# Optimization experiments

Hardware: AMD Instinct MI355X
Metric: run time of the kernel (lower is better)

Reference implementation:

```python
import jax, jax.numpy as jnp
import numpy as np

B, T, V = 128, 128, 30000
DE, DP, PV = 300, 30, 50
H = 300
HEADS = 6
LA, LL = 5, 24
POL = 3
RED = 10
NEG = -1e9


def entmax15(x):
    # exact 1.5-entmax along last axis (sorting algorithm, Peters & Martins 2019)
    d = x.shape[-1]
    x = x / 2.0
    x = x - jnp.max(x, axis=-1, keepdims=True)
    xs = -jnp.sort(-x, axis=-1)                      # descending
    rho = jnp.arange(1, d + 1, dtype=x.dtype)
    mean = jnp.cumsum(xs, axis=-1) / rho
    meansq = jnp.cumsum(xs * xs, axis=-1) / rho
    ss = rho * (meansq - mean * mean)
    delta = (1.0 - ss) / rho
    tau = mean - jnp.sqrt(jnp.maximum(delta, 0.0))
    support = jnp.sum((tau <= xs).astype(jnp.int32), axis=-1, keepdims=True)
    tau_star = jnp.take_along_axis(tau, support - 1, axis=-1)
    return jnp.square(jnp.maximum(x - tau_star, 0.0))


def lstm_dir(x, mask, Wih, Whh, bih, bhh, reverse):
    # packed-sequence-equivalent LSTM: state frozen / output zeroed at padded steps
    b = x.shape[0]
    h0 = jnp.zeros((b, Whh.shape[1]), x.dtype)

    def step(carry, inp):
        h, c = carry
        xt, mt = inp
        g = xt @ Wih.T + h @ Whh.T + (bih + bhh)
        i, f, gg, o = jnp.split(g, 4, axis=-1)       # torch gate order i,f,g,o
        c_new = jax.nn.sigmoid(f) * c + jax.nn.sigmoid(i) * jnp.tanh(gg)
        h_new = jax.nn.sigmoid(o) * jnp.tanh(c_new)
        m = mt[:, None]
        return (jnp.where(m, h_new, h), jnp.where(m, c_new, c)), jnp.where(m, h_new, 0.0)

    _, outs = jax.lax.scan(step, (h0, h0),
                           (jnp.swapaxes(x, 0, 1), jnp.swapaxes(mask, 0, 1)),
                           reverse=reverse)
    return jnp.swapaxes(outs, 0, 1)


def se_layer(x, valid, w1, b1, w2, b2):
    # SELayer over the SEQUENCE dim (channel == max_len); x: [b,t,d], valid: [b,t]
    y = jnp.mean(x, axis=-1)                         # adaptive avg-pool over (1, d)
    y = jax.nn.relu(y @ w1.T + b1) @ w2.T + b2
    y = y + jnp.where(valid > 0, 0.0, NEG)           # mask_2
    y = jax.nn.softmax(y, axis=1)
    return x * y[..., None]


def gcn(x, A, W, b):
    # D @ A @ D @ x @ W + b with D = diag((rowsum(A)+1)^-0.5)
    dn = (jnp.sum(A, axis=2) + 1.0) ** -0.5
    An = dn[:, :, None] * A * dn[:, None, :]
    return jnp.einsum('bij,bjd->bid', An, x) @ W + b


def _forward(text_indices, aspect_indices, left_indices, pos_indices, asp_post, height,
             adj, embed_matrix, pos_emb_w, Wih_f, Whh_f, bih_f, bhh_f,
             Wih_b, Whh_b, bih_b, bhh_b, wq, bq, wk, bk,
             se_w1, se_b1, se_w2, se_b2, gc1_w, gc1_b, gc2_w, gc2_b,
             affine1, affine2, fc_w, fc_b):
    b, t = text_indices.shape
    nonpad = text_indices != 0
    valid = nonpad.astype(jnp.float32)               # mask_ squeezed -> [b,t]
    text_len = jnp.sum(nonpad, axis=-1)
    aspect_real_len = jnp.sum(aspect_indices != 0, axis=-1)
    left_len = jnp.sum(left_indices != 0, axis=-1)   # aspect_double_idx = [left_len,left_len]

    # embedding; overwrite aspect position with mean aspect embedding
    text = embed_matrix[text_indices]
    am = (aspect_indices != 0).astype(jnp.float32)[..., None]
    asp_mean = jnp.sum(embed_matrix[aspect_indices] * am, axis=1) / aspect_real_len[:, None].astype(jnp.float32)
    text = text.at[jnp.arange(b), asp_post].set(asp_mean)
    embs = jnp.concatenate([text, pos_emb_w[pos_indices]], axis=-1)

    lenmask = jnp.arange(t)[None, :] < text_len[:, None]
    text_out = jnp.concatenate([
        lstm_dir(embs, lenmask, Wih_f, Whh_f, bih_f, bhh_f, False),
        lstm_dir(embs, lenmask, Wih_b, Whh_b, bih_b, bhh_b, True)], axis=-1)  # [b,t,2H]

    # multi-head entmax attention -> semantic adjacency
    dk = (2 * H) // HEADS
    q = (text_out @ wq.T + bq).reshape(b, t, HEADS, dk).transpose(0, 2, 1, 3)
    k = (text_out @ wk.T + bk).reshape(b, t, HEADS, dk).transpose(0, 2, 1, 3)
    scores = jnp.einsum('bhqd,bhkd->bhqk', q, k) / (dk ** 0.5)
    scores = jnp.where(nonpad[:, None, None, :], scores, NEG)
    adj_sem = jnp.mean(entmax15(scores), axis=1)     # average over heads
    eye = jnp.eye(t, dtype=adj_sem.dtype)
    adj_sem = adj_sem * (1.0 - eye) + eye            # zero diagonal, add identity
    adj_sem = valid[:, :, None] * adj_sem

    se = lambda z: se_layer(z, valid, se_w1, se_b1, se_w2, se_b2)
    # (the first x = relu(gc1(..,adj)); x = relu(gc2(..,adj)) branch is dead code:
    #  x is overwritten before use, so only the x_sem path matters)
    x_sem = jax.nn.relu(gcn(se(text_out), adj_sem, gc1_w, gc1_b))
    x = jax.nn.relu(gcn(se(x_sem), adj, gc2_w, gc2_b))

    A1 = jax.nn.softmax(jnp.einsum('bid,bjd->bij', x @ affine1, x_sem), axis=-1)
    A2 = jax.nn.softmax(jnp.einsum('bid,bjd->bij', x_sem @ affine2, x), axis=-1)
    out = jnp.concatenate([jnp.einsum('bij,bjd->bid', A1, x_sem),
                           jnp.einsum('bij,bjd->bid', A2, x)], axis=-1)  # [b,t,4H]
    aspmask = (jnp.arange(t)[None, :] == left_len[:, None]).astype(jnp.float32)
    pooled = jnp.sum(out * aspmask[..., None], axis=1)  # keep aspect token only
    return pooled @ fc_w + fc_b                         # [b, POL]


def setup_inputs():
    key = jax.random.key(0)
    ks = jax.random.split(key, 36)
    f32 = jnp.float32
    pos_t = jnp.arange(T)[None, :]
    text_len = jax.random.randint(ks[0], (B,), T // 2, T + 1)
    text_indices = jax.random.randint(ks[1], (B, T), 1, V) * (pos_t < text_len[:, None])
    asp_len = jax.random.randint(ks[2], (B,), 1, LA + 1)
    aspect_indices = jax.random.randint(ks[3], (B, LA), 1, V) * (jnp.arange(LA)[None, :] < asp_len[:, None])
    left_len = jax.random.randint(ks[4], (B,), 1, LL + 1)
    left_indices = jax.random.randint(ks[5], (B, LL), 1, V) * (jnp.arange(LL)[None, :] < left_len[:, None])
    pos_indices = jax.random.randint(ks[6], (B, T), 1, PV) * (pos_t < text_len[:, None])
    vmask = (pos_t < text_len[:, None]).astype(f32)
    adj = (jax.random.uniform(ks[7], (B, T, T)) < 0.08).astype(f32)
    adj = adj * vmask[:, :, None] * vmask[:, None, :]
    asp_post = left_len                              # aspect sits right after left context
    height = jax.random.randint(ks[8], (B, T + 1), 1, 12)

    def rn(k, shape, scale=0.05):
        return jax.random.normal(k, shape, dtype=f32) * scale

    params = dict(
        embed_matrix=rn(ks[9], (V, DE), 0.5),
        pos_emb_w=rn(ks[10], (PV, DP), 0.5).at[0].set(0.0),
        Wih_f=rn(ks[11], (4 * H, DE + DP)), Whh_f=rn(ks[12], (4 * H, H)),
        bih_f=rn(ks[13], (4 * H,)), bhh_f=rn(ks[14], (4 * H,)),
        Wih_b=rn(ks[15], (4 * H, DE + DP)), Whh_b=rn(ks[16], (4 * H, H)),
        bih_b=rn(ks[17], (4 * H,)), bhh_b=rn(ks[18], (4 * H,)),
        wq=rn(ks[19], (2 * H, 2 * H)), bq=rn(ks[20], (2 * H,)),
        wk=rn(ks[21], (2 * H, 2 * H)), bk=rn(ks[22], (2 * H,)),
        se_w1=rn(ks[23], (T // RED, T)), se_b1=rn(ks[24], (T // RED,)),
        se_w2=rn(ks[25], (T, T // RED)), se_b2=rn(ks[26], (T,)),
        gc1_w=rn(ks[27], (2 * H, 2 * H)), gc1_b=rn(ks[28], (2 * H,)),
        gc2_w=rn(ks[29], (2 * H, 2 * H)), gc2_b=rn(ks[30], (2 * H,)),
        affine1=rn(ks[31], (2 * H, 2 * H)), affine2=rn(ks[32], (2 * H, 2 * H)),
        fc_w=rn(ks[33], (4 * H, POL)), fc_b=rn(ks[34], (POL,)),
    )
    return dict(text_indices=text_indices, aspect_indices=aspect_indices,
                left_indices=left_indices, pos_indices=pos_indices,
                asp_post=asp_post, height=height, adj=adj, **params)


def reference(text_indices, aspect_indices, left_indices, pos_indices, asp_post, height,
              adj, embed_matrix, pos_emb_w, Wih_f, Whh_f, bih_f, bhh_f,
              Wih_b, Whh_b, bih_b, bhh_b, wq, bq, wk, bk,
              se_w1, se_b1, se_w2, se_b2, gc1_w, gc1_b, gc2_w, gc2_b,
              affine1, affine2, fc_w, fc_b):
    return _forward(text_indices, aspect_indices, left_indices, pos_indices, asp_post, height,
                    adj, embed_matrix, pos_emb_w, Wih_f, Whh_f, bih_f, bhh_f,
                    Wih_b, Whh_b, bih_b, bhh_b, wq, bq, wk, bk,
                    se_w1, se_b1, se_w2, se_b2, gc1_w, gc1_b, gc2_w, gc2_b,
                    affine1, affine2, fc_w, fc_b)
```

## Files before the change

kernel.cpp:

```cpp
#include <hip/hip_runtime.h>

typedef unsigned short ushort_t;
typedef unsigned int   uint_t;
typedef __attribute__((ext_vector_type(8))) short short8;
typedef __attribute__((ext_vector_type(4))) float floatx4;

#define NEGV -1000000000.0f

__device__ __forceinline__ float bf2f(ushort_t h){ return __uint_as_float(((uint_t)h)<<16); }
__device__ __forceinline__ ushort_t f2bf(float f){
  uint_t u = __float_as_uint(f);
  uint_t r = u + 0x7fffu + ((u>>16)&1u);
  return (ushort_t)(r>>16);
}
__device__ __forceinline__ float wredsum(float v){ for(int o=32;o;o>>=1) v += __shfl_xor(v,o); return v; }
__device__ __forceinline__ float wredmax(float v){ for(int o=32;o;o>>=1) v = fmaxf(v,__shfl_xor(v,o)); return v; }
__device__ __forceinline__ int   wredsumi(int v){ for(int o=32;o;o>>=1) v += __shfl_xor(v,o); return v; }

__device__ __forceinline__ short8 ldg_cohr(const ushort_t* p){
  short8 r;
  asm volatile("global_load_dwordx4 %0, %1, off sc0 sc1"
               : "=&v"(r) : "v"(p) : "memory");
  return r;
}
__device__ __forceinline__ void stg_b128_cohr(ushort_t* p, short8 v){
  asm volatile("global_store_dwordx4 %0, %1, off sc0 sc1" :: "v"(p), "v"(v) : "memory");
}

__device__ __forceinline__ float fsig(float x){ return 1.f/(1.f+__expf(-x)); }
__device__ __forceinline__ float ftanh(float x){ return 1.f - 2.f/(1.f+__expf(2.f*x)); }

__global__ void k_cvt8(const void* __restrict__ src, ushort_t* __restrict__ dst,
                       long n, const ushort_t* __restrict__ probe_src){
  __shared__ int sflag;
  if (threadIdx.x < 64){
    ushort_t u = probe_src[2*threadIdx.x];
    int e = (u>>7)&0xFF;
    int c = (e>=100 && e<=140) ? 1 : 0;
    c = wredsumi(c);
    if (threadIdx.x==0) sflag = (c>32) ? 1 : 0;
  }
  __syncthreads();
  bool isbf = (sflag!=0);
  long base = (blockIdx.x*256L + threadIdx.x)*8;
  if (base>=n) return;
  if (isbf){
    if (base+8<=n) *(uint4*)(dst+base) = *(const uint4*)((const ushort_t*)src+base);
    else for (long i=base;i<n;i++) dst[i]=((const ushort_t*)src)[i];
  } else {
    const float* s = (const float*)src;
    if (base+8<=n){
      float4 v0 = *(const float4*)(s+base);
      float4 v1 = *(const float4*)(s+base+4);
      ushort_t o[8] = {f2bf(v0.x),f2bf(v0.y),f2bf(v0.z),f2bf(v0.w),
                       f2bf(v1.x),f2bf(v1.y),f2bf(v1.z),f2bf(v1.w)};
      *(uint4*)(dst+base) = *(uint4*)o;
    } else {
      for (long i=base;i<n;i++) dst[i]=f2bf(s[i]);
    }
  }
}

__device__ __forceinline__ bool probe_is_bf16(const ushort_t* probe_src){
  int c=0;
  #pragma unroll 1
  for (int i=0;i<64;i++){
    ushort_t u = probe_src[2*i];
    int e = (u>>7)&0xFF;
    c += (e>=100 && e<=140) ? 1 : 0;
  }
  return c>32;
}

__global__ void k_lens(const int* __restrict__ ti, const int* __restrict__ li,
                       int* __restrict__ nonpad, int* __restrict__ text_len,
                       int* __restrict__ left_len){
  int b = blockIdx.x, t = threadIdx.x;
  nonpad[b*128+t] = (ti[b*128+t]!=0) ? 1 : 0;
  if (t==0){
    int c=0; for (int k2=0;k2<128;k2++) c += (ti[b*128+k2]!=0);
    text_len[b]=c;
    int l=0; for (int k2=0;k2<24;k2++) l += (li[b*24+k2]!=0);
    left_len[b]=l;
  }
}

__global__ void k_aspmean(const int* __restrict__ ai, const ushort_t* __restrict__ em,
                          float* __restrict__ asp_mean){
  int b = blockIdx.x;
  int idxs[5]; int cnt=0;
  for (int a=0;a<5;a++){ int ix=ai[b*5+a]; idxs[a]=ix; cnt += (ix!=0); }
  float inv = 1.0f/(float)cnt;
  for (int d=threadIdx.x; d<300; d+=128){
    float s=0.f;
    for (int a=0;a<5;a++) if (idxs[a]) s += bf2f(em[(long)idxs[a]*300+d]);
    asp_mean[b*300+d] = s*inv;
  }
}

__global__ void k_embs(const int* __restrict__ ti, const int* __restrict__ pi,
                       const int* __restrict__ asp_post,
                       const ushort_t* __restrict__ em, const ushort_t* __restrict__ pe,
                       const float* __restrict__ asp_mean, ushort_t* __restrict__ embs){
  int blk = blockIdx.x;
  int b = blk>>7, t = blk&127;
  int ap = asp_post[b];
  int tix = ti[b*128+t];
  int pix = pi[b*128+t];
  for (int col=threadIdx.x; col<336; col+=128){
    ushort_t v;
    if (col<300) v = (t==ap) ? f2bf(asp_mean[b*300+col]) : em[(long)tix*300+col];
    else if (col<330) v = pe[pix*30 + (col-300)];
    else v = 0;
    embs[(long)(b*128+t)*336 + col] = v;
  }
}

__global__ void k_padwih2(const ushort_t* __restrict__ src, ushort_t* __restrict__ dst){
  int i = blockIdx.x*blockDim.x + threadIdx.x;
  if (i >= 1280*336) return;
  int r = i/336, k = i - r*336;
  int j = r>>2, gate = r&3;
  ushort_t v = 0;
  if (j<300 && k<330) v = src[(long)(gate*300+j)*330 + k];
  dst[i] = v;
}

__global__ void k_padwhh2(const ushort_t* __restrict__ src, ushort_t* __restrict__ dst){
  int i = blockIdx.x*blockDim.x + threadIdx.x;
  if (i >= 1280*320) return;
  int r = i/320, k = i - r*320;
  int j = r>>2, gate = r&3;
  ushort_t v = 0;
  if (j<300 && k<300) v = src[(long)(gate*300+j)*300 + k];
  dst[i] = v;
}

__global__ void k_biassum2(const ushort_t* __restrict__ a, const ushort_t* __restrict__ b,
                           float* __restrict__ dst){
  int i = blockIdx.x*blockDim.x + threadIdx.x;
  if (i>=1280) return;
  int j = i>>2, g = i&3;
  dst[i] = (j<300) ? (bf2f(a[g*300+j]) + bf2f(b[g*300+j])) : 0.f;
}

__global__ void k_biascvt(const ushort_t* __restrict__ a, float* __restrict__ dst, int n){
  int i = blockIdx.x*blockDim.x + threadIdx.x;
  if (i<n) dst[i] = bf2f(a[i]);
}

template<int TB, int MODE>
__global__ __launch_bounds__(256) void gemm_k(
    int M, int N, int K,
    const ushort_t* __restrict__ A, long lda, long sAz,
    const ushort_t* __restrict__ B, long ldb, long sBz,
    float* __restrict__ Cf, ushort_t* __restrict__ Cb, long ldc, long sCz,
    const float* __restrict__ bias, int relu,
    const float* __restrict__ rowscale,
    const int* __restrict__ nonpad)
{
  __shared__ ushort_t As[128*40];
  __shared__ ushort_t Bs[128*40];
  const int tid = threadIdx.x;
  const int m0 = blockIdx.x*128, n0 = blockIdx.y*128;
  const int z = blockIdx.z;
  const ushort_t* Ap = A + (long)z*sAz;
  const ushort_t* Bp = B + (long)z*sBz;
  floatx4 acc[4][4];
  #pragma unroll
  for (int i=0;i<4;i++)
    #pragma unroll
    for (int j=0;j<4;j++){ acc[i][j][0]=0.f; acc[i][j][1]=0.f; acc[i][j][2]=0.f; acc[i][j][3]=0.f; }
  const int w = tid>>6, wm = w&1, wn = w>>1;
  const int lane = tid&63, lr = lane&15, lq = lane>>4;

  for (int k0=0;k0<K;k0+=32){
    #pragma unroll
    for (int c2=0;c2<2;c2++){
      int ch = tid + 256*c2;
      int row = ch>>2, kc = (ch&3)*8;
      int gr = m0+row, gk = k0+kc;
      uint4 v{};
      if (gr<M && gk<K) v = *(const uint4*)(Ap + (long)gr*lda + gk);
      *(uint4*)(&As[row*40+kc]) = v;
    }
    if (TB){
      #pragma unroll
      for (int c2=0;c2<2;c2++){
        int ch = tid + 256*c2;
        int row = ch>>2, kc = (ch&3)*8;
        int gn = n0+row, gk = k0+kc;
        uint4 v{};
        if (gn<N && gk<K) v = *(const uint4*)(Bp + (long)gn*ldb + gk);
        int sw = kc ^ (((row>>3)&3)<<3);
        *(uint4*)(&Bs[row*40+sw]) = v;
      }
    } else {
      #pragma unroll
      for (int c2=0;c2<2;c2++){
        int ch = tid + 256*c2;
        int kk = ch>>4, nc = (ch&15)*8;
        int gk = k0+kk, gn = n0+nc;
        uint4 v{};
        if (gk<K && gn<N) v = *(const uint4*)(Bp + (long)gk*ldb + gn);
        uint_t wsv[4] = {v.x, v.y, v.z, v.w};
        #pragma unroll
        for (int e=0;e<8;e++){
          ushort_t hv = (e&1) ? (ushort_t)(wsv[e>>1]>>16) : (ushort_t)(wsv[e>>1]&0xffffu);
          int n = nc+e;
          int sw = kk ^ (((n>>3)&3)<<3);
          Bs[n*40+sw] = hv;
        }
      }
    }
    __syncthreads();
    short8 af[4], bfv[4];
    #pragma unroll
    for (int i=0;i<4;i++) af[i] = *(const short8*)(&As[(wm*64+i*16+lr)*40 + lq*8]);
    #pragma unroll
    for (int j=0;j<4;j++){
      int n = wn*64+j*16+lr;
      int sw = (lq*8) ^ (((n>>3)&3)<<3);
      bfv[j] = *(const short8*)(&Bs[n*40+sw]);
    }
    #pragma unroll
    for (int i=0;i<4;i++)
      #pragma unroll
      for (int j=0;j<4;j++)
        acc[i][j] = __builtin_amdgcn_mfma_f32_16x16x32_bf16(af[i], bfv[j], acc[i][j], 0,0,0);
    __syncthreads();
  }

  #pragma unroll
  for (int i=0;i<4;i++){
    #pragma unroll
    for (int j=0;j<4;j++){
      #pragma unroll
      for (int r=0;r<4;r++){
        int row = m0 + wm*64 + i*16 + lq*4 + r;
        int col = n0 + wn*64 + j*16 + lr;
        if (row<M && col<N){
          float v = acc[i][j][r];
          if (rowscale) v *= rowscale[(long)z*M + row];
          if (bias) v += bias[col];
          if (relu && v<0.f) v = 0.f;
          if (MODE==1){
            Cb[(long)z*sCz + (long)row*ldc + col] = f2bf(v);
          } else if (MODE==2){
            int b = row>>7, t = row&127;
            int h = col/100, d = col - h*100;
            Cb[ ((long)((b*6+h)*128+t))*104 + d ] = f2bf(v);
          } else if (MODE==3){
            v *= 0.1f;
            if (!nonpad[(z/6)*128 + col]) v = NEGV;
            Cf[(long)z*sCz + (long)row*ldc + col] = v;
          }
        }
      }
    }
  }
}

#define BLD 328
#define HXD 40

__global__ __launch_bounds__(512,1) void lstm2_k(
    const ushort_t* __restrict__ whh2f, const ushort_t* __restrict__ whh2b,
    const ushort_t* __restrict__ gipf, const ushort_t* __restrict__ gipb,
    ushort_t* __restrict__ hbuf,
    int* __restrict__ barr,
    ushort_t* __restrict__ text_out, const int* __restrict__ text_len,
    ushort_t* __restrict__ dumpb)
{
  __shared__ ushort_t Blds[64*BLD];
  __shared__ ushort_t hx[64*HXD];

  const int bx = blockIdx.x;
  const int slice = bx % 10;
  const int grp   = bx / 10;
  const int dir = grp & 1, bh = grp >> 1;
  const ushort_t* __restrict__ whh = dir ? whh2b : whh2f;
  const ushort_t* __restrict__ gip = dir ? gipb : gipf;
  ushort_t* hb = hbuf + (long)dir * (2L*128*320);
  int* bar = barr + grp*128;

  const int tid = threadIdx.x;
  const int w = tid>>6, lane = tid&63, lr = lane&15, lq = lane>>4;
  const int wm = w&3, wn = w>>2;

  short8 a[2][10];
  #pragma unroll
  for (int mi=0;mi<2;mi++){
    const ushort_t* ar = whh + (long)(slice*128 + (wm*2+mi)*16 + lr)*320 + lq*8;
    #pragma unroll
    for (int kf=0;kf<10;kf++) a[mi][kf] = *(const short8*)(ar + kf*32);
  }
  #pragma unroll
  for (int mi=0;mi<2;mi++)
    #pragma unroll
    for (int kf=0;kf<10;kf++)
      asm volatile("" : "+v"(a[mi][kf]));

  int jj_[2], b_[2], bl_[2], tl_[2];
  #pragma unroll
  for (int mi=0;mi<2;mi++) jj_[mi] = slice*32 + wm*8 + mi*4 + lq;
  #pragma unroll
  for (int ni=0;ni<2;ni++){
    bl_[ni] = wn*32 + ni*16 + lr;
    b_[ni]  = bh*64 + bl_[ni];
    tl_[ni] = text_len[b_[ni]];
  }

  const int boff0 = (wn*32+   lr)*BLD + lq*8;
  const int boff1 = (wn*32+16+lr)*BLD + lq*8;

  float    c_st[2][2];
  ushort_t h_st[2][2];
  #pragma unroll
  for (int mi=0;mi<2;mi++){ c_st[mi][0]=0.f; c_st[mi][1]=0.f; h_st[mi][0]=0; h_st[mi][1]=0; }

  uint2 gp[2][2];
  {
    int t0 = dir ? 127 : 0;
    #pragma unroll
    for (int mi=0;mi<2;mi++)
      #pragma unroll
      for (int ni=0;ni<2;ni++)
        gp[mi][ni] = *(const uint2*)(gip + ((long)(b_[ni]*128 + t0))*1280 + jj_[mi]*4);
  }

  for (int s=0; s<128; s++){
    const int t = dir ? (127-s) : s;
    const ushort_t* rb = hb + (long)(s&1)*(128L*320);
    ushort_t*       wb = hb + (long)((s+1)&1)*(128L*320);

    short8 tmp[5]; int ro_[5], ch_[5];
    #pragma unroll
    for (int k=0;k<5;k++){
      int c = tid + k*512;
      int row = c/40, ch = c - row*40;
      ro_[k]=row; ch_[k]=ch;
      tmp[k] = ldg_cohr(rb + (long)(bh*64+row)*320 + ch*8);
    }
    asm volatile("s_waitcnt vmcnt(0)" ::: "memory");
    __builtin_amdgcn_sched_barrier(0);
    #pragma unroll
    for (int k=0;k<5;k++)
      *(short8*)(&Blds[ro_[k]*BLD + ch_[k]*8]) = tmp[k];
    __syncthreads();

    floatx4 acc[2][2];
    #pragma unroll
    for (int mi=0;mi<2;mi++)
      #pragma unroll
      for (int ni=0;ni<2;ni++){ acc[mi][ni][0]=0.f; acc[mi][ni][1]=0.f; acc[mi][ni][2]=0.f; acc[mi][ni][3]=0.f; }
    #pragma unroll
    for (int kf=0;kf<10;kf++){
      short8 b0 = *(const short8*)(&Blds[boff0 + kf*32]);
      short8 b1 = *(const short8*)(&Blds[boff1 + kf*32]);
      acc[0][0] = __builtin_amdgcn_mfma_f32_16x16x32_bf16(a[0][kf], b0, acc[0][0], 0,0,0);
      acc[0][1] = __builtin_amdgcn_mfma_f32_16x16x32_bf16(a[0][kf], b1, acc[0][1], 0,0,0);
      acc[1][0] = __builtin_amdgcn_mfma_f32_16x16x32_bf16(a[1][kf], b0, acc[1][0], 0,0,0);
      acc[1][1] = __builtin_amdgcn_mfma_f32_16x16x32_bf16(a[1][kf], b1, acc[1][1], 0,0,0);
    }

    ushort_t tov[2][2];
    #pragma unroll
    for (int mi=0;mi<2;mi++){
      #pragma unroll
      for (int ni=0;ni<2;ni++){
        float g_i = acc[mi][ni][0] + bf2f((ushort_t)(gp[mi][ni].x & 0xffffu));
        float g_f = acc[mi][ni][1] + bf2f((ushort_t)(gp[mi][ni].x >> 16));
        float g_g = acc[mi][ni][2] + bf2f((ushort_t)(gp[mi][ni].y & 0xffffu));
        float g_o = acc[mi][ni][3] + bf2f((ushort_t)(gp[mi][ni].y >> 16));
        float ig = fsig(g_i);
        float fg = fsig(g_f);
        float gg = ftanh(g_g);
        float og = fsig(g_o);
        float cn = fg*c_st[mi][ni] + ig*gg;
        float hn = og*ftanh(cn);
        bool m = (t < tl_[ni]);
        if (m) c_st[mi][ni] = cn;
        ushort_t hv = m ? f2bf(hn) : h_st[mi][ni];
        h_st[mi][ni] = hv;
        hx[bl_[ni]*HXD + wm*8 + mi*4 + lq] = hv;
        tov[mi][ni] = m ? f2bf(hn) : (ushort_t)0;
      }
    }
    __syncthreads();

    if (tid < 256){
      int row = tid>>2, jj8 = (tid&3)*8;
      short8 hvv = *(const short8*)(&hx[row*HXD + jj8]);
      stg_b128_cohr(wb + (long)(bh*64+row)*320 + slice*32 + jj8, hvv);
    }
    #pragma unroll
    for (int mi=0;mi<2;mi++)
      #pragma unroll
      for (int ni=0;ni<2;ni++){
        ushort_t* toa = (jj_[mi] < 300)
          ? &text_out[((long)(b_[ni]*128 + t))*600 + dir*300 + jj_[mi]]
          : &dumpb[tid*4 + mi*2 + ni];
        *toa = tov[mi][ni];
      }
    {
      int tn = dir ? ((s<127) ? (126-s) : 127) : ((s<127) ? (s+1) : 0);
      #pragma unroll
      for (int mi=0;mi<2;mi++)
        #pragma unroll
        for (int ni=0;ni<2;ni++)
          gp[mi][ni] = *(const uint2*)(gip + ((long)(b_[ni]*128 + tn))*1280 + jj_[mi]*4);
    }
    asm volatile("s_waitcnt vmcnt(8)" ::: "memory");
    __syncthreads();
    if (tid==0){
      __hip_atomic_fetch_add(&bar[s], 1, __ATOMIC_RELAXED, __HIP_MEMORY_SCOPE_AGENT);
      while (__hip_atomic_load(&bar[s], __ATOMIC_RELAXED, __HIP_MEMORY_SCOPE_AGENT) < 10)
        __builtin_amdgcn_s_sleep(1);
    }
    __syncthreads();
  }
}

__global__ __launch_bounds__(64) void k_entmax(float* __restrict__ p){
  long row = blockIdx.x;
  float* base = p + row*128;
  __shared__ float xo[128], xs[128], c1[128], c2[128];
  int t = threadIdx.x;
  float a = base[t]*0.5f, b = base[t+64]*0.5f;
  float m = wredmax(fmaxf(a,b));
  a -= m; b -= m;
  xo[t]=a; xo[t+64]=b; xs[t]=a; xs[t+64]=b;
  __syncthreads();
  for (int k2=2;k2<=128;k2<<=1){
    for (int j=k2>>1;j>0;j>>=1){
      int i = ((t & ~(j-1))<<1) | (t & (j-1));
      int ixj = i | j;
      float vi = xs[i], vj = xs[ixj];
      bool blk = (i & k2)==0;
      bool sw = blk ? (vi < vj) : (vi > vj);
      __syncthreads();
      if (sw){ xs[i]=vj; xs[ixj]=vi; }
      __syncthreads();
    }
  }
  c1[t]=xs[t];       c2[t]=xs[t]*xs[t];
  c1[t+64]=xs[t+64]; c2[t+64]=xs[t+64]*xs[t+64];
  __syncthreads();
  for (int d=1; d<128; d<<=1){
    float a1 = (t>=d)     ? c1[t-d]    : 0.f;
    float a2 = (t>=d)     ? c2[t-d]    : 0.f;
    float b1 = (t+64>=d)  ? c1[t+64-d] : 0.f;
    float b2 = (t+64>=d)  ? c2[t+64-d] : 0.f;
    float x1=c1[t], y1=c2[t], x2=c1[t+64], y2=c2[t+64];
    __syncthreads();
    c1[t]=x1+a1; c2[t]=y1+a2; c1[t+64]=x2+b1; c2[t+64]=y2+b2;
    __syncthreads();
  }
  float tau_a, tau_b; int cnt=0;
  {
    float rho = (float)(t+1);
    float mean = c1[t]/rho, msq = c2[t]/rho;
    float ss = rho*(msq-mean*mean);
    float delta = (1.f-ss)/rho;
    tau_a = mean - sqrtf(fmaxf(delta,0.f));
    cnt += (tau_a <= xs[t]) ? 1 : 0;
  }
  {
    float rho = (float)(t+65);
    float mean = c1[t+64]/rho, msq = c2[t+64]/rho;
    float ss = rho*(msq-mean*mean);
    float delta = (1.f-ss)/rho;
    tau_b = mean - sqrtf(fmaxf(delta,0.f));
    cnt += (tau_b <= xs[t+64]) ? 1 : 0;
  }
  __syncthreads();
  c1[t]=tau_a; c1[t+64]=tau_b;
  __syncthreads();
  int support = wredsumi(cnt);
  support = (support<1) ? 1 : ((support>128) ? 128 : support);
  float tau_star = c1[support-1];
  float oa = fmaxf(xo[t]-tau_star, 0.f);
  float ob = fmaxf(xo[t+64]-tau_star, 0.f);
  base[t] = oa*oa; base[t+64] = ob*ob;
}

__global__ void k_adjsem(const float* __restrict__ p, const int* __restrict__ nonpad,
                         ushort_t* __restrict__ adj_sem){
  int idx = blockIdx.x*blockDim.x + threadIdx.x;
  if (idx >= 128*128*128) return;
  int b = idx>>14, rem = idx&16383, i = rem>>7, j = rem&127;
  float s = 0.f;
  for (int h=0;h<6;h++) s += p[(long)b*98304 + h*16384 + i*128 + j];
  float v = s/6.0f;
  if (i==j) v = 1.0f;
  if (!nonpad[b*128+i]) v = 0.f;
  adj_sem[idx] = f2bf(v);
}

__global__ __launch_bounds__(64) void k_dn(const ushort_t* __restrict__ src, float* __restrict__ dnv){
  long row = blockIdx.x;
  int l = threadIdx.x;
  float s = bf2f(src[row*128+l]) + bf2f(src[row*128+l+64]);
  s = wredsum(s);
  if (l==0) dnv[row] = 1.0f/sqrtf(s+1.0f);
}

__global__ __launch_bounds__(64) void k_mean(const ushort_t* __restrict__ X, float* __restrict__ ymean){
  long row = blockIdx.x;
  float s=0.f;
  for (int d=threadIdx.x; d<600; d+=64) s += bf2f(X[row*600+d]);
  s = wredsum(s);
  if (threadIdx.x==0) ymean[row] = s/600.0f;
}

__global__ void k_senet(const float* __restrict__ ymean,
                        const ushort_t* __restrict__ w1, const ushort_t* __restrict__ b1,
                        const ushort_t* __restrict__ w2, const ushort_t* __restrict__ b2,
                        const int* __restrict__ nonpad, float* __restrict__ ysoft){
  int b = blockIdx.x, t = threadIdx.x;
  __shared__ float yv[128], z1[12], red[128];
  yv[t] = ymean[b*128+t];
  __syncthreads();
  if (t<12){
    float s = bf2f(b1[t]);
    for (int k2=0;k2<128;k2++) s += yv[k2]*bf2f(w1[t*128+k2]);
    z1[t] = fmaxf(s,0.f);
  }
  __syncthreads();
  float v = bf2f(b2[t]);
  for (int r=0;r<12;r++) v += z1[r]*bf2f(w2[t*12+r]);
  if (!nonpad[b*128+t]) v += NEGV;
  red[t]=v; __syncthreads();
  for (int s2=64;s2>0;s2>>=1){ if (t<s2) red[t]=fmaxf(red[t],red[t+s2]); __syncthreads(); }
  float mx = red[0]; __syncthreads();
  float e = expf(v-mx);
  red[t]=e; __syncthreads();
  for (int s2=64;s2>0;s2>>=1){ if (t<s2) red[t]+=red[t+s2]; __syncthreads(); }
  float sm = red[0];
  ysoft[b*128+t] = e/sm;
}

__global__ void k_scale2(const ushort_t* __restrict__ X, const float* __restrict__ ysoft,
                         const float* __restrict__ dnv, ushort_t* __restrict__ out){
  int i = blockIdx.x*blockDim.x + threadIdx.x;
  if (i >= 128*128*600) return;
  int row = i/600;
  out[i] = f2bf(bf2f(X[i])*ysoft[row]*dnv[row]);
}

__global__ void k_gather(const ushort_t* __restrict__ X, const int* __restrict__ left_len,
                         ushort_t* __restrict__ dst){
  int b = blockIdx.x;
  int lb = left_len[b];
  for (int d=threadIdx.x; d<600; d+=128)
    dst[b*600+d] = X[(long)(b*128+lb)*600+d];
}

__global__ __launch_bounds__(256) void k_pool(const ushort_t* __restrict__ g,
                                              const ushort_t* __restrict__ X,
                                              float* __restrict__ pooled, int poff){
  int b = blockIdx.x, tid = threadIdx.x;
  __shared__ float gs[600], sbuf[128], red[256];
  for (int d=tid; d<600; d+=256) gs[d] = bf2f(g[b*600+d]);
  __syncthreads();
  int wv = tid>>6, lane = tid&63;
  for (int jj=wv; jj<128; jj+=4){
    float s=0.f;
    for (int d=lane; d<600; d+=64) s += gs[d]*bf2f(X[(long)(b*128+jj)*600+d]);
    s = wredsum(s);
    if (lane==0) sbuf[jj]=s;
  }
  __syncthreads();
  float v = (tid<128) ? sbuf[tid] : -3.4e38f;
  red[tid]=v; __syncthreads();
  for (int s2=128;s2>0;s2>>=1){ if (tid<s2) red[tid]=fmaxf(red[tid],red[tid+s2]); __syncthreads(); }
  float mx = red[0]; __syncthreads();
  float e = (tid<128) ? expf(v-mx) : 0.f;
  red[tid]=e; __syncthreads();
  for (int s2=128;s2>0;s2>>=1){ if (tid<s2) red[tid]+=red[tid+s2]; __syncthreads(); }
  float sm = red[0]; __syncthreads();
  if (tid<128) sbuf[tid] = e/sm;
  __syncthreads();
  for (int d=tid; d<600; d+=256){
    float acc=0.f;
    for (int j=0;j<128;j++) acc += sbuf[j]*bf2f(X[(long)(b*128+j)*600+d]);
    pooled[(long)b*1200 + poff + d] = acc;
  }
}

__global__ __launch_bounds__(64) void k_final(const float* __restrict__ pooled,
                                              const ushort_t* __restrict__ fcw,
                                              const ushort_t* __restrict__ fcb,
                                              void* __restrict__ out,
                                              const ushort_t* __restrict__ probe_src){
  bool isbf = probe_is_bf16(probe_src);
  int b = blockIdx.x, lane = threadIdx.x;
  for (int p=0;p<3;p++){
    float s=0.f;
    for (int d=lane; d<1200; d+=64) s += pooled[(long)b*1200+d]*bf2f(fcw[d*3+p]);
    s = wredsum(s);
    if (lane==0){
      float r = s + bf2f(fcb[p]);
      if (isbf) ((ushort_t*)out)[b*3+p] = f2bf(r);
      else      ((float*)out)[b*3+p] = r;
    }
  }
}

extern "C" void kernel_launch(void* const* d_in, const int* in_sizes, int n_in,
                              void* d_out, int out_size, void* d_ws, size_t ws_size,
                              hipStream_t stream) {
  const int*      ti   = (const int*)d_in[0];
  const int*      ai   = (const int*)d_in[1];
  const int*      li   = (const int*)d_in[2];
  const int*      pi   = (const int*)d_in[3];
  const int*      aps  = (const int*)d_in[4];
  const ushort_t* probe = (const ushort_t*)d_in[7];

  char* w = (char*)d_ws; size_t off = 0;
  auto alloc = [&](size_t bytes)->char*{ char* p = w+off; off = (off+bytes+255)&~(size_t)255; return p; };

  int*   text_len = (int*)alloc(512);
  int*   left_len = (int*)alloc(512);
  int*   nonpad   = (int*)alloc(65536);
  float* asp_mean = (float*)alloc(153600);
  float* dn1      = (float*)alloc(65536);
  float* dn2      = (float*)alloc(65536);
  float* ymean    = (float*)alloc(65536);
  float* ysoft    = (float*)alloc(65536);
  ushort_t* wihpf = (ushort_t*)alloc(860160);
  ushort_t* wihpb = (ushort_t*)alloc(860160);
  ushort_t* whh2f = (ushort_t*)alloc(819200);
  ushort_t* whh2b = (ushort_t*)alloc(819200);
  ushort_t* hbuf  = (ushort_t*)alloc(327680);
  int*      barr  = (int*)alloc(2048);
  ushort_t* dumpb = (ushort_t*)alloc(4096);
  float* biasgf   = (float*)alloc(5120);
  float* biasgb   = (float*)alloc(5120);
  float* bqf      = (float*)alloc(2400);
  float* bkf      = (float*)alloc(2400);
  float* gc1bf    = (float*)alloc(2400);
  float* gc2bf    = (float*)alloc(2400);
  ushort_t* g1    = (ushort_t*)alloc(153600);
  ushort_t* g2    = (ushort_t*)alloc(153600);
  ushort_t* xr    = (ushort_t*)alloc(153600);
  ushort_t* xsr   = (ushort_t*)alloc(153600);
  float* pooled   = (float*)alloc(614400);
  ushort_t* adj_c  = (ushort_t*)alloc(4194304);
  ushort_t* pe_c   = (ushort_t*)alloc(2048);
  ushort_t* wihf_c = (ushort_t*)alloc(792000);
  ushort_t* wihb_c = (ushort_t*)alloc(792000);
  ushort_t* whhf_c = (ushort_t*)alloc(720000);
  ushort_t* whhb_c = (ushort_t*)alloc(720000);
  ushort_t* bihf_c = (ushort_t*)alloc(2400);
  ushort_t* bhhf_c = (ushort_t*)alloc(2400);
  ushort_t* bihb_c = (ushort_t*)alloc(2400);
  ushort_t* bhhb_c = (ushort_t*)alloc(2400);
  ushort_t* wq_c   = (ushort_t*)alloc(720000);
  ushort_t* bq_c   = (ushort_t*)alloc(1200);
  ushort_t* wk_c   = (ushort_t*)alloc(720000);
  ushort_t* bk_c   = (ushort_t*)alloc(1200);
  ushort_t* sw1_c  = (ushort_t*)alloc(3072);
  ushort_t* sb1_c  = (ushort_t*)alloc(256);
  ushort_t* sw2_c  = (ushort_t*)alloc(3072);
  ushort_t* sb2_c  = (ushort_t*)alloc(256);
  ushort_t* g1w_c  = (ushort_t*)alloc(720000);
  ushort_t* g1b_c  = (ushort_t*)alloc(1200);
  ushort_t* g2w_c  = (ushort_t*)alloc(720000);
  ushort_t* g2b_c  = (ushort_t*)alloc(1200);
  ushort_t* af1_c  = (ushort_t*)alloc(720000);
  ushort_t* af2_c  = (ushort_t*)alloc(720000);
  ushort_t* fcw_c  = (ushort_t*)alloc(7200);
  ushort_t* fcb_c  = (ushort_t*)alloc(256);
  ushort_t* embs  = (ushort_t*)alloc(11010048);
  ushort_t* textout = (ushort_t*)alloc(19660800);
  char* R = alloc(95420416);
  ushort_t* em_c    = (ushort_t*)(R);
  ushort_t* gip_f   = (ushort_t*)(R);
  ushort_t* gip_b   = (ushort_t*)(R+41943040);
  ushort_t* qh      = (ushort_t*)(R);
  ushort_t* kh      = (ushort_t*)(R+20447232);
  float*    scores  = (float*)(R+40894464);
  ushort_t* adj_sem = (ushort_t*)(R+91226112);
  ushort_t* se_x    = (ushort_t*)(R+40894464);
  ushort_t* Zb      = (ushort_t*)(R+60555264);
  ushort_t* x_sem   = (ushort_t*)(R);
  ushort_t* xb      = (ushort_t*)(R+20447232);
  (void)ws_size; (void)n_in; (void)in_sizes; (void)out_size;

  {
    const int idx[27] = {7,6, 8,9,13,10,14,11,12,15,16,17,18,19,20,21,22,23,24,25,26,27,28,29,30,31,32};
    ushort_t* dl[27] = {em_c,adj_c, pe_c,wihf_c,wihb_c,whhf_c,whhb_c,bihf_c,bhhf_c,bihb_c,bhhb_c,
                        wq_c,bq_c,wk_c,bk_c,sw1_c,sb1_c,sw2_c,sb2_c,
                        g1w_c,g1b_c,g2w_c,g2b_c,af1_c,af2_c,fcw_c,fcb_c};
    const long nl[27] = {9000000L,2097152L, 900,396000,396000,360000,360000,1200,1200,1200,1200,
                         360000,600,360000,600,1536,12,1536,128,
                         360000,600,360000,600,360000,360000,3600,3};
    for (int i=0;i<27;i++){
      long nb = ((nl[i]+7)/8 + 255)/256;
      k_cvt8<<<(int)nb,256,0,stream>>>(d_in[idx[i]], dl[i], nl[i], probe);
    }
  }

  k_lens<<<128,128,0,stream>>>(ti, li, nonpad, text_len, left_len);
  k_aspmean<<<128,128,0,stream>>>(ai, em_c, asp_mean);
  k_embs<<<16384,128,0,stream>>>(ti, pi, aps, em_c, pe_c, asp_mean, embs);
  k_padwih2<<<(1280*336+255)/256,256,0,stream>>>(wihf_c, wihpf);
  k_padwih2<<<(1280*336+255)/256,256,0,stream>>>(wihb_c, wihpb);
  k_padwhh2<<<(1280*320+255)/256,256,0,stream>>>(whhf_c, whh2f);
  k_padwhh2<<<(1280*320+255)/256,256,0,stream>>>(whhb_c, whh2b);
  k_biassum2<<<(1280+255)/256,256,0,stream>>>(bihf_c, bhhf_c, biasgf);
  k_biassum2<<<(1280+255)/256,256,0,stream>>>(bihb_c, bhhb_c, biasgb);
  k_biascvt<<<3,256,0,stream>>>(bq_c, bqf, 600);
  k_biascvt<<<3,256,0,stream>>>(bk_c, bkf, 600);
  k_biascvt<<<3,256,0,stream>>>(g1b_c, gc1bf, 600);
  k_biascvt<<<3,256,0,stream>>>(g2b_c, gc2bf, 600);

  gemm_k<1,1><<<dim3(128,10,1),256,0,stream>>>(16384,1280,336, embs,336,0, wihpf,336,0,
        nullptr, gip_f,1280,0, biasgf,0,nullptr,nullptr);
  gemm_k<1,1><<<dim3(128,10,1),256,0,stream>>>(16384,1280,336, embs,336,0, wihpb,336,0,
        nullptr, gip_b,1280,0, biasgb,0,nullptr,nullptr);

  hipMemsetAsync(hbuf, 0, 327680, stream);
  hipMemsetAsync(barr, 0, 2048, stream);
  lstm2_k<<<40,512,0,stream>>>(whh2f, whh2b, gip_f, gip_b, hbuf, barr, textout, text_len, dumpb);

  hipMemsetAsync(qh, 0, 20447232, stream);
  hipMemsetAsync(kh, 0, 20447232, stream);
  gemm_k<1,2><<<dim3(128,5,1),256,0,stream>>>(16384,600,600, textout,600,0, wq_c,600,0,
        nullptr, qh,0,0, bqf,0,nullptr,nullptr);
  gemm_k<1,2><<<dim3(128,5,1),256,0,stream>>>(16384,600,600, textout,600,0, wk_c,600,0,
        nullptr, kh,0,0, bkf,0,nullptr,nullptr);

  gemm_k<1,3><<<dim3(1,1,768),256,0,stream>>>(128,128,104, qh,104,13312, kh,104,13312,
        scores, nullptr, 128, 16384, nullptr,0,nullptr, nonpad);

  k_entmax<<<98304,64,0,stream>>>(scores);

  k_adjsem<<<(2097152+255)/256,256,0,stream>>>(scores, nonpad, adj_sem);
  k_dn<<<16384,64,0,stream>>>(adj_sem, dn1);
  k_dn<<<16384,64,0,stream>>>(adj_c, dn2);

  k_mean<<<16384,64,0,stream>>>(textout, ymean);
  k_senet<<<128,128,0,stream>>>(ymean, sw1_c,sb1_c,sw2_c,sb2_c, nonpad, ysoft);
  k_scale2<<<(9830400+255)/256,256,0,stream>>>(textout, ysoft, dn1, se_x);
  gemm_k<0,1><<<dim3(1,5,128),256,0,stream>>>(128,600,128, adj_sem,128,16384, se_x,600,76800,
        nullptr, Zb,600,76800, nullptr,0, dn1, nullptr);
  gemm_k<0,1><<<dim3(128,5,1),256,0,stream>>>(16384,600,600, Zb,600,0, g1w_c,600,0,
        nullptr, x_sem,600,0, gc1bf,1,nullptr,nullptr);

  k_mean<<<16384,64,0,stream>>>(x_sem, ymean);
  k_senet<<<128,128,0,stream>>>(ymean, sw1_c,sb1_c,sw2_c,sb2_c, nonpad, ysoft);
  k_scale2<<<(9830400+255)/256,256,0,stream>>>(x_sem, ysoft, dn2, se_x);
  gemm_k<0,1><<<dim3(1,5,128),256,0,stream>>>(128,600,128, adj_c,128,16384, se_x,600,76800,
        nullptr, Zb,600,76800, nullptr,0, dn2, nullptr);
  gemm_k<0,1><<<dim3(128,5,1),256,0,stream>>>(16384,600,600, Zb,600,0, g2w_c,600,0,
        nullptr, xb,600,0, gc2bf,1,nullptr,nullptr);

  k_gather<<<128,128,0,stream>>>(xb, left_len, xr);
  k_gather<<<128,128,0,stream>>>(x_sem, left_len, xsr);
  gemm_k<0,1><<<dim3(1,5,1),256,0,stream>>>(128,600,600, xr,600,0, af1_c,600,0,
        nullptr, g1,600,0, nullptr,0,nullptr,nullptr);
  gemm_k<0,1><<<dim3(1,5,1),256,0,stream>>>(128,600,600, xsr,600,0, af2_c,600,0,
        nullptr, g2,600,0, nullptr,0,nullptr,nullptr);
  k_pool<<<128,256,0,stream>>>(g1, x_sem, pooled, 0);
  k_pool<<<128,256,0,stream>>>(g2, xb, pooled, 600);

  k_final<<<128,64,0,stream>>>(pooled, fcw_c, fcb_c, d_out, probe);
}
```

Baseline: 1.865 ms.

## Batch small weight conversions, use per-slice flags for LSTM barrier, zero only pad columns

Merges 25 small conversion launches into one multi-tensor kernel indexed by blockIdx.y. The LSTM inter-block barrier changes from an atomic counter polled by thread 0 plus a second syncthreads to per-slice flag stores that every wave polls directly. The full memsets of the q/k head buffers are replaced by a kernel that zeroes only the four pad columns per row. The aims are fewer launches, lower per-step barrier latency in the recurrent loop, and less memset traffic. The risk is that waves polling independently read h before the other slices have published it, if memory ordering is not preserved.

```diff
diff --git a/kernel.cpp b/kernel.cpp
--- a/kernel.cpp
+++ b/kernel.cpp
@@ -61,6 +61,42 @@
   }
 }
 
+struct CvtTab { const void* src[25]; ushort_t* dst[25]; long n[25]; };
+
+__global__ void k_cvt8_multi(CvtTab tab, const ushort_t* __restrict__ probe_src){
+  __shared__ int sflag;
+  if (threadIdx.x < 64){
+    ushort_t u = probe_src[2*threadIdx.x];
+    int e = (u>>7)&0xFF;
+    int c = (e>=100 && e<=140) ? 1 : 0;
+    c = wredsumi(c);
+    if (threadIdx.x==0) sflag = (c>32) ? 1 : 0;
+  }
+  __syncthreads();
+  bool isbf = (sflag!=0);
+  int ix = blockIdx.y;
+  long n = tab.n[ix];
+  long base = (blockIdx.x*256L + threadIdx.x)*8;
+  if (base>=n) return;
+  const void* src = tab.src[ix];
+  ushort_t* dst = tab.dst[ix];
+  if (isbf){
+    if (base+8<=n) *(uint4*)(dst+base) = *(const uint4*)((const ushort_t*)src+base);
+    else for (long i=base;i<n;i++) dst[i]=((const ushort_t*)src)[i];
+  } else {
+    const float* s = (const float*)src;
+    if (base+8<=n){
+      float4 v0 = *(const float4*)(s+base);
+      float4 v1 = *(const float4*)(s+base+4);
+      ushort_t o[8] = {f2bf(v0.x),f2bf(v0.y),f2bf(v0.z),f2bf(v0.w),
+                       f2bf(v1.x),f2bf(v1.y),f2bf(v1.z),f2bf(v1.w)};
+      *(uint4*)(dst+base) = *(uint4*)o;
+    } else {
+      for (long i=base;i<n;i++) dst[i]=f2bf(s[i]);
+    }
+  }
+}
+
 __device__ __forceinline__ bool probe_is_bf16(const ushort_t* probe_src){
   int c=0;
   #pragma unroll 1
@@ -147,6 +183,15 @@
 __global__ void k_biascvt(const ushort_t* __restrict__ a, float* __restrict__ dst, int n){
   int i = blockIdx.x*blockDim.x + threadIdx.x;
   if (i<n) dst[i] = bf2f(a[i]);
+}
+
+__global__ void k_padzero(ushort_t* __restrict__ qh, ushort_t* __restrict__ kh){
+  int i = blockIdx.x*blockDim.x + threadIdx.x;
+  if (i >= 98304*4*2) return;
+  int half = (i >= 98304*4) ? 1 : 0;
+  int j = i - half*98304*4;
+  int row = j>>2, c = 100 + (j&3);
+  (half ? kh : qh)[(long)row*104 + c] = 0;
 }
 
 template<int TB, int MODE>
@@ -282,7 +327,7 @@
   const ushort_t* __restrict__ whh = dir ? whh2b : whh2f;
   const ushort_t* __restrict__ gip = dir ? gipb : gipf;
   ushort_t* hb = hbuf + (long)dir * (2L*128*320);
-  int* bar = barr + grp*128;
+  int* flg = barr + grp*160;
 
   const int tid = threadIdx.x;
   const int w = tid>>6, lane = tid&63, lr = lane&15, lq = lane>>4;
@@ -413,12 +458,19 @@
     }
     asm volatile("s_waitcnt vmcnt(8)" ::: "memory");
     __syncthreads();
-    if (tid==0){
-      __hip_atomic_fetch_add(&bar[s], 1, __ATOMIC_RELAXED, __HIP_MEMORY_SCOPE_AGENT);
-      while (__hip_atomic_load(&bar[s], __ATOMIC_RELAXED, __HIP_MEMORY_SCOPE_AGENT) < 10)
-        __builtin_amdgcn_s_sleep(1);
-    }
-    __syncthreads();
+
+    if (tid==0)
+      __hip_atomic_store(&flg[slice*16], s+1, __ATOMIC_RELAXED, __HIP_MEMORY_SCOPE_AGENT);
+    {
+      bool done = false;
+      do {
+        int f = 0x7fffffff;
+        if (lane < 10)
+          f = __hip_atomic_load(&flg[lane*16], __ATOMIC_RELAXED, __HIP_MEMORY_SCOPE_AGENT);
+        done = (bool)__all(f >= s+1);
+        if (!done) __builtin_amdgcn_s_sleep(1);
+      } while(!done);
+    }
   }
 }
 
@@ -634,7 +686,7 @@
   ushort_t* whh2f = (ushort_t*)alloc(819200);
   ushort_t* whh2b = (ushort_t*)alloc(819200);
   ushort_t* hbuf  = (ushort_t*)alloc(327680);
-  int*      barr  = (int*)alloc(2048);
+  int*      barr  = (int*)alloc(4096);
   ushort_t* dumpb = (ushort_t*)alloc(4096);
   float* biasgf   = (float*)alloc(5120);
   float* biasgb   = (float*)alloc(5120);
@@ -689,18 +741,19 @@
   ushort_t* xb      = (ushort_t*)(R+20447232);
   (void)ws_size; (void)n_in; (void)in_sizes; (void)out_size;
 
+  k_cvt8<<<(9000000/8+255)/256,256,0,stream>>>(d_in[7], em_c, 9000000L, probe);
+  k_cvt8<<<(2097152/8+255)/256,256,0,stream>>>(d_in[6], adj_c, 2097152L, probe);
   {
-    const int idx[27] = {7,6, 8,9,13,10,14,11,12,15,16,17,18,19,20,21,22,23,24,25,26,27,28,29,30,31,32};
-    ushort_t* dl[27] = {em_c,adj_c, pe_c,wihf_c,wihb_c,whhf_c,whhb_c,bihf_c,bhhf_c,bihb_c,bhhb_c,
+    CvtTab tab;
+    const int idx[25] = {8,9,13,10,14,11,12,15,16,17,18,19,20,21,22,23,24,25,26,27,28,29,30,31,32};
+    ushort_t* dl[25] = {pe_c,wihf_c,wihb_c,whhf_c,whhb_c,bihf_c,bhhf_c,bihb_c,bhhb_c,
                         wq_c,bq_c,wk_c,bk_c,sw1_c,sb1_c,sw2_c,sb2_c,
                         g1w_c,g1b_c,g2w_c,g2b_c,af1_c,af2_c,fcw_c,fcb_c};
-    const long nl[27] = {9000000L,2097152L, 900,396000,396000,360000,360000,1200,1200,1200,1200,
+    const long nl[25] = {900,396000,396000,360000,360000,1200,1200,1200,1200,
                          360000,600,360000,600,1536,12,1536,128,
                          360000,600,360000,600,360000,360000,3600,3};
-    for (int i=0;i<27;i++){
-      long nb = ((nl[i]+7)/8 + 255)/256;
-      k_cvt8<<<(int)nb,256,0,stream>>>(d_in[idx[i]], dl[i], nl[i], probe);
-    }
+    for (int i=0;i<25;i++){ tab.src[i]=d_in[idx[i]]; tab.dst[i]=dl[i]; tab.n[i]=nl[i]; }
+    k_cvt8_multi<<<dim3(194,25),256,0,stream>>>(tab, probe);
   }
 
   k_lens<<<128,128,0,stream>>>(ti, li, nonpad, text_len, left_len);
@@ -723,11 +776,10 @@
         nullptr, gip_b,1280,0, biasgb,0,nullptr,nullptr);
 
   hipMemsetAsync(hbuf, 0, 327680, stream);
-  hipMemsetAsync(barr, 0, 2048, stream);
+  hipMemsetAsync(barr, 0, 4096, stream);
   lstm2_k<<<40,512,0,stream>>>(whh2f, whh2b, gip_f, gip_b, hbuf, barr, textout, text_len, dumpb);
 
-  hipMemsetAsync(qh, 0, 20447232, stream);
-  hipMemsetAsync(kh, 0, 20447232, stream);
+  k_padzero<<<(98304*4*2+255)/256,256,0,stream>>>(qh, kh);
   gemm_k<1,2><<<dim3(128,5,1),256,0,stream>>>(16384,600,600, textout,600,0, wq_c,600,0,
         nullptr, qh,0,0, bqf,0,nullptr,nullptr);
   gemm_k<1,2><<<dim3(128,5,1),256,0,stream>>>(16384,600,600, textout,600,0, wk_c,600,0,
```

Result: faster. 1.793 ms (-3.9%).
